# Optimization experiments

Hardware: AMD Instinct MI355X
Metric: run time of the kernel (lower is better)

## Reference

```python
import jax, jax.numpy as jnp
import numpy as np

EPS = 1e-7        # keras backend.epsilon()
TEMPERATURE = 0.1
MOMENTUM = 0.9
CENTROID_LR = 0.1
REPULSION_STRENGTH = 0.1
MIN_DISTANCE = 1.0

B, S, D = 8, 4096, 512
K = 512


def setup_inputs() -> dict:
    key = jax.random.key(0)
    kx, kc = jax.random.split(key)
    x = jax.random.normal(kx, (B, S, D), dtype=jnp.float32)
    # GlorotNormal for (K, D) centroid table
    glorot_std = float(np.sqrt(2.0 / (K + D)))
    centroids = jax.random.normal(kc, (K, D), dtype=jnp.float32) * glorot_std
    centroid_momentum = jnp.zeros((K, D), dtype=jnp.float32)
    return {"x": x, "centroids": centroids, "centroid_momentum": centroid_momentum}


def reference(x, centroids, centroid_momentum):
    # ---- flatten non-feature dims: (B, S, D) -> (N, D) ----
    flat = x.reshape(-1, x.shape[-1])                      # (N, D)

    # ---- squared Euclidean distances to centroids (GEMM form) ----
    x_sq = jnp.sum(flat * flat, axis=-1, keepdims=True)    # (N, 1)
    c_sq = jnp.sum(centroids * centroids, axis=-1)         # (K,)
    cross = flat @ centroids.T                             # (N, K)
    distances = x_sq + c_sq[None, :] - 2.0 * cross         # (N, K)

    # ---- temperature-scaled soft assignments (stable softmax w/ eps) ----
    scaled = -distances / TEMPERATURE
    scaled = scaled - jnp.max(scaled, axis=-1, keepdims=True)
    exp_d = jnp.exp(scaled)
    assignments = exp_d / (jnp.sum(exp_d, axis=-1, keepdims=True) + EPS)  # (N, K)

    # ---- soft K-means centroid targets ----
    sum_w = jnp.sum(assignments, axis=0)                   # (K,)
    weighted_sum = assignments.T @ flat                    # (K, D)
    new_centroids = weighted_sum / (sum_w[:, None] + EPS)  # (K, D)

    # ---- pairwise centroid repulsion ----
    diffs = centroids[:, None, :] - centroids[None, :, :]  # (K, K, D)
    sq_dist = jnp.sum(diffs * diffs, axis=-1)              # (K, K)
    dist = jnp.sqrt(sq_dist + EPS)
    rep_w = jnp.maximum(0.0, 1.0 - dist / MIN_DISTANCE)
    rep_scale = (REPULSION_STRENGTH * rep_w / (dist + EPS))[..., None]
    repulsion = jnp.sum(rep_scale * diffs, axis=1)         # (K, D)

    # ---- momentum update of centroids ----
    updates = new_centroids - centroids + repulsion
    mom_new = MOMENTUM * centroid_momentum + (1.0 - MOMENTUM) * updates
    centroids_new = centroids + CENTROID_LR * mom_new

    # ---- output: assignments reshaped to (B, S, K) ----
    out = assignments.reshape(x.shape[:-1] + (assignments.shape[-1],))
    return out, centroids_new, mom_new
```

## Files before the change

kernel.cpp:

```cpp
#include <hip/hip_runtime.h>
#include <hip/hip_bf16.h>

#define EPSF 1e-7f

typedef __attribute__((ext_vector_type(8))) short bf16x8;
typedef __attribute__((ext_vector_type(4))) float f32x4v;

__device__ inline ushort f2bf_bits(float x) {
    union { __hip_bfloat16 b; ushort u; } cv;
    cv.b = __float2bfloat16(x);
    return cv.u;
}
__device__ inline float bfbits2f(ushort u) {
    union { ushort u; __hip_bfloat16 b; } cv;
    cv.u = u;
    return __bfloat162float(cv.b);
}
__device__ inline void split2(float x, ushort& h, ushort& l) {
    h = f2bf_bits(x);
    l = f2bf_bits(x - bfbits2f(h));
}
__device__ inline uint4 pack8(const ushort* h) {
    uint4 p;
    p.x = (uint)h[0] | ((uint)h[1] << 16);
    p.y = (uint)h[2] | ((uint)h[3] << 16);
    p.z = (uint)h[4] | ((uint)h[5] << 16);
    p.w = (uint)h[6] | ((uint)h[7] << 16);
    return p;
}

__device__ inline void gload_lds16(const ushort* g, ushort* l) {
    __builtin_amdgcn_global_load_lds(
        (const __attribute__((address_space(1))) unsigned int*)g,
        (__attribute__((address_space(3))) unsigned int*)l, 16, 0, 0);
}

__global__ __launch_bounds__(256) void csqc_v3(const float* __restrict__ C,
                                               float* __restrict__ csq,
                                               ushort* __restrict__ Chl) {
    const int wave = threadIdx.x >> 6, lane = threadIdx.x & 63;
    const int row = blockIdx.x * 4 + wave;
    const int kc = lane >> 2, s = lane & 3;
    const float* p = C + row * 512 + lane * 8;
    float4 a = *(const float4*)p;
    float4 b = *(const float4*)(p + 4);
    float v[8] = {a.x, a.y, a.z, a.w, b.x, b.y, b.z, b.w};
    ushort h[8], l[8];
    float sqs = 0.f;
#pragma unroll
    for (int i = 0; i < 8; ++i) {
        sqs += v[i] * v[i];
        split2(v[i], h[i], l[i]);
    }
    ushort* base = Chl + (long)row * 1024 + kc * 64 + s * 8;
    *(uint4*)base = pack8(h);
    *(uint4*)(base + 32) = pack8(l);
#pragma unroll
    for (int off = 1; off < 64; off <<= 1) sqs += __shfl_xor(sqs, off, 64);
    if (lane == 0) csq[row] = sqs;
}

__global__ __launch_bounds__(512) void logsm(const float* __restrict__ X,
                                             const ushort* __restrict__ Chl,
                                             const float* __restrict__ csq,
                                             float* __restrict__ assign,
                                             ushort* __restrict__ Abf,
                                             ushort* __restrict__ Xh,
                                             float* __restrict__ sum_w) {
    __shared__ __align__(16) ushort sA[64 * 64];
    __shared__ __align__(16) ushort sB[512 * 64];
    __shared__ float rmaxs[64][4];
    __shared__ float rsums[64][4];
    __shared__ float swacc[512];
    const int tid = threadIdx.x;
    const int m0 = ((blockIdx.x & 7) * 64 + (blockIdx.x >> 3)) * 64;
    const int wid = tid >> 6, lane = tid & 63;
    const int wm = wid >> 2, wn = wid & 3;
    const int lrow = lane & 15, lkb = lane >> 4;
    swacc[tid] = 0.f;
    f32x4v acc[2][8] = {};

    const int ar = tid >> 3, aq = tid & 7;

#pragma unroll 1
    for (int kc = 0; kc < 16; ++kc) {
        __syncthreads();
        {
            float4 v = *(const float4*)(X + (long)(m0 + ar) * 512 + kc * 32 + aq * 4);
            ushort h[4], l[4];
            split2(v.x, h[0], l[0]);
            split2(v.y, h[1], l[1]);
            split2(v.z, h[2], l[2]);
            split2(v.w, h[3], l[3]);
            ushort4 hv = {h[0], h[1], h[2], h[3]};
            ushort4 lv = {l[0], l[1], l[2], l[3]};
            const int sh = (aq >> 1) ^ (ar & 7);
            const int slo = ((aq >> 1) + 4) ^ (ar & 7);
            *(ushort4*)&sA[ar * 64 + (sh << 3) + (aq & 1) * 4] = hv;
            *(ushort4*)&sA[ar * 64 + (slo << 3) + (aq & 1) * 4] = lv;
            *(ushort4*)(Xh + (long)(m0 + ar) * 512 + kc * 32 + aq * 4) = hv;
        }
#pragma unroll
        for (int i = 0; i < 8; ++i) {
            const int sl = i * 512 + tid;
            const int r = sl >> 3, j = sl & 7;
            const int s = j ^ (r & 7);
            gload_lds16(Chl + (long)r * 1024 + kc * 64 + s * 8,
                        &sB[(i * 512 + wid * 64) * 8]);
        }
        __syncthreads();
        bf16x8 ah[2], al[2];
#pragma unroll
        for (int mi = 0; mi < 2; ++mi) {
            const int R = wm * 32 + mi * 16 + lrow;
            ah[mi] = *(const bf16x8*)&sA[R * 64 + ((lkb ^ (R & 7)) << 3)];
            al[mi] = *(const bf16x8*)&sA[R * 64 + (((lkb + 4) ^ (R & 7)) << 3)];
        }
#pragma unroll
        for (int ni = 0; ni < 8; ++ni) {
            const int Rn = wn * 128 + ni * 16 + lrow;
            bf16x8 bh = *(const bf16x8*)&sB[Rn * 64 + ((lkb ^ (Rn & 7)) << 3)];
            bf16x8 bl = *(const bf16x8*)&sB[Rn * 64 + (((lkb + 4) ^ (Rn & 7)) << 3)];
#pragma unroll
            for (int mi = 0; mi < 2; ++mi) {
                acc[mi][ni] = __builtin_amdgcn_mfma_f32_16x16x32_bf16(ah[mi], bh, acc[mi][ni], 0, 0, 0);
                acc[mi][ni] = __builtin_amdgcn_mfma_f32_16x16x32_bf16(ah[mi], bl, acc[mi][ni], 0, 0, 0);
                acc[mi][ni] = __builtin_amdgcn_mfma_f32_16x16x32_bf16(al[mi], bh, acc[mi][ni], 0, 0, 0);
            }
        }
    }
    const int colb = wn * 128 + lrow;
    float cs[8];
#pragma unroll
    for (int ni = 0; ni < 8; ++ni) cs[ni] = csq[colb + ni * 16];
    float mx[2][4];
#pragma unroll
    for (int mi = 0; mi < 2; ++mi)
#pragma unroll
        for (int r = 0; r < 4; ++r) {
            float m = -3.0e38f;
#pragma unroll
            for (int ni = 0; ni < 8; ++ni) {
                float l = 2.0f * acc[mi][ni][r] - cs[ni];
                acc[mi][ni][r] = l;
                m = fmaxf(m, l);
            }
            mx[mi][r] = m;
        }
#pragma unroll
    for (int off = 1; off < 16; off <<= 1)
#pragma unroll
        for (int mi = 0; mi < 2; ++mi)
#pragma unroll
            for (int r = 0; r < 4; ++r) mx[mi][r] = fmaxf(mx[mi][r], __shfl_xor(mx[mi][r], off, 64));
    if (lrow == 0) {
#pragma unroll
        for (int mi = 0; mi < 2; ++mi)
#pragma unroll
            for (int r = 0; r < 4; ++r) rmaxs[wm * 32 + mi * 16 + lkb * 4 + r][wn] = mx[mi][r];
    }
    __syncthreads();
    float gmax[2][4];
#pragma unroll
    for (int mi = 0; mi < 2; ++mi)
#pragma unroll
        for (int r = 0; r < 4; ++r) {
            const int row = wm * 32 + mi * 16 + lkb * 4 + r;
            gmax[mi][r] = fmaxf(fmaxf(rmaxs[row][0], rmaxs[row][1]),
                                fmaxf(rmaxs[row][2], rmaxs[row][3]));
        }
    float sm[2][4] = {};
#pragma unroll
    for (int mi = 0; mi < 2; ++mi)
#pragma unroll
        for (int ni = 0; ni < 8; ++ni)
#pragma unroll
            for (int r = 0; r < 4; ++r) {
                float e = expf((acc[mi][ni][r] - gmax[mi][r]) * 10.0f);
                acc[mi][ni][r] = e;
                sm[mi][r] += e;
            }
#pragma unroll
    for (int off = 1; off < 16; off <<= 1)
#pragma unroll
        for (int mi = 0; mi < 2; ++mi)
#pragma unroll
            for (int r = 0; r < 4; ++r) sm[mi][r] += __shfl_xor(sm[mi][r], off, 64);
    if (lrow == 0) {
#pragma unroll
        for (int mi = 0; mi < 2; ++mi)
#pragma unroll
            for (int r = 0; r < 4; ++r) rsums[wm * 32 + mi * 16 + lkb * 4 + r][wn] = sm[mi][r];
    }
    __syncthreads();
    float inv[2][4];
#pragma unroll
    for (int mi = 0; mi < 2; ++mi)
#pragma unroll
        for (int r = 0; r < 4; ++r) {
            const int row = wm * 32 + mi * 16 + lkb * 4 + r;
            float t = rsums[row][0] + rsums[row][1] + rsums[row][2] + rsums[row][3];
            inv[mi][r] = 1.0f / (t + EPSF);
        }
    float csum[8] = {};
#pragma unroll
    for (int mi = 0; mi < 2; ++mi)
#pragma unroll
        for (int ni = 0; ni < 8; ++ni) {
            const int col = colb + ni * 16;
#pragma unroll
            for (int r = 0; r < 4; ++r) {
                const int row = wm * 32 + mi * 16 + lkb * 4 + r;
                float a = acc[mi][ni][r] * inv[mi][r];
                assign[(long)(m0 + row) * 512 + col] = a;
                Abf[(long)(m0 + row) * 512 + col] = f2bf_bits(a);
                csum[ni] += a;
            }
        }
#pragma unroll
    for (int off = 16; off < 64; off <<= 1)
#pragma unroll
        for (int ni = 0; ni < 8; ++ni) csum[ni] += __shfl_xor(csum[ni], off, 64);
    if (lkb == 0) {
#pragma unroll
        for (int ni = 0; ni < 8; ++ni) atomicAdd(&swacc[colb + ni * 16], csum[ni]);
    }
    __syncthreads();
    atomicAdd(&sum_w[tid], swacc[tid]);
}

__global__ __launch_bounds__(256) void gram_s_v3(const ushort* __restrict__ Chl,
                                                 const float* __restrict__ csq,
                                                 float* __restrict__ S,
                                                 float* __restrict__ rsum) {
    __shared__ __align__(16) ushort sA[128 * 64];
    __shared__ __align__(16) ushort sB[128 * 64];
    __shared__ float rs_s[128];
    const int tid = threadIdx.x;
    const int n0 = blockIdx.x * 128;
    const int m0 = blockIdx.y * 128;
    const int wid = tid >> 6, lane = tid & 63;
    const int wm = wid >> 1, wn = wid & 1;
    const int lrow = lane & 15, lkb = lane >> 4;
    f32x4v acc[4][4] = {};

#pragma unroll 1
    for (int kc = 0; kc < 16; ++kc) {
        __syncthreads();
#pragma unroll
        for (int i = 0; i < 4; ++i) {
            const int sl = wid * 256 + i * 64 + lane;
            const int r = sl >> 3, j = sl & 7;
            const int s = j ^ (r & 7);
            gload_lds16(Chl + (long)(m0 + r) * 1024 + kc * 64 + s * 8,
                        &sA[(wid * 256 + i * 64) * 8]);
            gload_lds16(Chl + (long)(n0 + r) * 1024 + kc * 64 + s * 8,
                        &sB[(wid * 256 + i * 64) * 8]);
        }
        __syncthreads();
        bf16x8 ah[4], al[4], bh[4], bl[4];
#pragma unroll
        for (int mi = 0; mi < 4; ++mi) {
            const int R = wm * 64 + mi * 16 + lrow;
            ah[mi] = *(const bf16x8*)&sA[R * 64 + ((lkb ^ (R & 7)) << 3)];
            al[mi] = *(const bf16x8*)&sA[R * 64 + (((lkb + 4) ^ (R & 7)) << 3)];
        }
#pragma unroll
        for (int ni = 0; ni < 4; ++ni) {
            const int R = wn * 64 + ni * 16 + lrow;
            bh[ni] = *(const bf16x8*)&sB[R * 64 + ((lkb ^ (R & 7)) << 3)];
            bl[ni] = *(const bf16x8*)&sB[R * 64 + (((lkb + 4) ^ (R & 7)) << 3)];
        }
#pragma unroll
        for (int mi = 0; mi < 4; ++mi)
#pragma unroll
            for (int ni = 0; ni < 4; ++ni) {
                acc[mi][ni] = __builtin_amdgcn_mfma_f32_16x16x32_bf16(ah[mi], bh[ni], acc[mi][ni], 0, 0, 0);
                acc[mi][ni] = __builtin_amdgcn_mfma_f32_16x16x32_bf16(ah[mi], bl[ni], acc[mi][ni], 0, 0, 0);
                acc[mi][ni] = __builtin_amdgcn_mfma_f32_16x16x32_bf16(al[mi], bh[ni], acc[mi][ni], 0, 0, 0);
            }
    }
    if (tid < 128) rs_s[tid] = 0.f;
    __syncthreads();
    const int colb = n0 + wn * 64 + lrow;
    float csj[4];
#pragma unroll
    for (int ni = 0; ni < 4; ++ni) csj[ni] = csq[colb + ni * 16];
#pragma unroll
    for (int mi = 0; mi < 4; ++mi) {
        const int rowb = m0 + wm * 64 + mi * 16 + lkb * 4;
#pragma unroll
        for (int r = 0; r < 4; ++r) {
            const int row = rowb + r;
            const float csi = csq[row];
            float rowpart = 0.f;
#pragma unroll
            for (int ni = 0; ni < 4; ++ni) {
                const int col = colb + ni * 16;
                float sq = csi + csj[ni] - 2.0f * acc[mi][ni][r];
                float dist = sqrtf(fmaxf(sq, 0.f) + EPSF);
                float w = fmaxf(0.f, 1.f - dist);
                float sval = (row == col) ? 0.f : (0.1f * w / (dist + EPSF));
                S[(long)row * 512 + col] = sval;
                rowpart += sval;
            }
            atomicAdd(&rs_s[row - m0], rowpart);
        }
    }
    __syncthreads();
    if (tid < 128) atomicAdd(&rsum[m0 + tid], rs_s[tid]);
}

__global__ __launch_bounds__(256) void wsum_v3(const ushort* __restrict__ Abf,
                                               const ushort* __restrict__ Xh,
                                               float* __restrict__ WSp) {
    __shared__ __align__(16) ushort sA[128 * 64];
    __shared__ __align__(16) ushort sB[128 * 64];
    const int tid = threadIdx.x;
    const int lin = blockIdx.x + blockIdx.y * 4 + blockIdx.z * 16;
    const int T = (lin & 7) * 64 + (lin >> 3);
    const int k0 = (T & 3) * 128;
    const int d0 = ((T >> 2) & 3) * 128;
    const int zc = T >> 4;
    const long n0 = (long)zc * 1024;
    const int wid = tid >> 6, lane = tid & 63;
    const int wm = wid >> 1, wn = wid & 1;
    const int lrow = lane & 15, lkb = lane >> 4;
    f32x4v acc[4][4] = {};

    for (int nc = 0; nc < 1024; nc += 64) {
        __syncthreads();
#pragma unroll
        for (int it = 0; it < 4; ++it) {
            const int idx = it * 256 + tid;
            const int c = idx & 127;
            const int no = idx >> 7;
            const long nb = n0 + nc + (long)no * 8;
            const int dd = d0 + c;
            ushort ha[8], hx[8];
#pragma unroll
            for (int jj = 0; jj < 8; ++jj) {
                ha[jj] = Abf[(nb + jj) * 512 + k0 + c];
                hx[jj] = Xh[(nb + jj) * 512 + dd];
            }
            const int sl = no ^ (c & 7);
            *(uint4*)&sA[c * 64 + sl * 8] = pack8(ha);
            *(uint4*)&sB[c * 64 + sl * 8] = pack8(hx);
        }
        __syncthreads();
#pragma unroll
        for (int kk = 0; kk < 2; ++kk) {
            const int j = kk * 4 + lkb;
            bf16x8 af[4], bfv[4];
#pragma unroll
            for (int mi = 0; mi < 4; ++mi) {
                const int R = wm * 64 + mi * 16 + lrow;
                af[mi] = *(const bf16x8*)&sA[R * 64 + ((j ^ (R & 7)) << 3)];
            }
#pragma unroll
            for (int ni = 0; ni < 4; ++ni) {
                const int R = wn * 64 + ni * 16 + lrow;
                bfv[ni] = *(const bf16x8*)&sB[R * 64 + ((j ^ (R & 7)) << 3)];
            }
#pragma unroll
            for (int mi = 0; mi < 4; ++mi)
#pragma unroll
                for (int ni = 0; ni < 4; ++ni)
                    acc[mi][ni] = __builtin_amdgcn_mfma_f32_16x16x32_bf16(af[mi], bfv[ni], acc[mi][ni], 0, 0, 0);
        }
    }
    float* dst = WSp + (size_t)zc * 262144;
#pragma unroll
    for (int mi = 0; mi < 4; ++mi) {
        const int k = k0 + wm * 64 + mi * 16 + lkb * 4;
#pragma unroll
        for (int ni = 0; ni < 4; ++ni) {
            const int d = d0 + wn * 64 + ni * 16 + lrow;
#pragma unroll
            for (int r = 0; r < 4; ++r)
                dst[(k + r) * 512 + d] = acc[mi][ni][r];
        }
    }
}

__global__ __launch_bounds__(256) void apply_update(const float* __restrict__ Cent,
                                                    const float* __restrict__ Mom,
                                                    const float* __restrict__ S,
                                                    const float* __restrict__ rsum,
                                                    const float* __restrict__ WSp,
                                                    const float* __restrict__ sum_w,
                                                    float* __restrict__ outC,
                                                    float* __restrict__ outM) {
    const int i = blockIdx.x;
    __shared__ float srow[512];
    __shared__ int nz;
    const int tid = threadIdx.x;
    if (tid == 0) nz = 0;
    __syncthreads();
    float2 sv = *(const float2*)(S + (long)i * 512 + tid * 2);
    srow[tid * 2] = sv.x;
    srow[tid * 2 + 1] = sv.y;
    if (sv.x != 0.f || sv.y != 0.f) nz = 1;
    __syncthreads();
    const float rs = rsum[i];
    const float invw = 1.0f / (sum_w[i] + EPSF);
    const int d0 = tid * 2;
    float ws0 = 0.f, ws1 = 0.f;
#pragma unroll 4
    for (int z = 0; z < 32; ++z) {
        float2 w = *(const float2*)(WSp + (size_t)z * 262144 + (long)i * 512 + d0);
        ws0 += w.x;
        ws1 += w.y;
    }
    float sc0 = 0.f, sc1 = 0.f;
    if (nz) {
        for (int j = 0; j < 512; ++j) {
            const float s = srow[j];
            if (s != 0.f) {
                sc0 += s * Cent[(long)j * 512 + d0];
                sc1 += s * Cent[(long)j * 512 + d0 + 1];
            }
        }
    }
    float2 ci = *(const float2*)(Cent + (long)i * 512 + d0);
    float2 mo = *(const float2*)(Mom + (long)i * 512 + d0);
    float rep0 = rs * ci.x - sc0;
    float rep1 = rs * ci.y - sc1;
    float mn0 = 0.9f * mo.x + 0.1f * (ws0 * invw - ci.x + rep0);
    float mn1 = 0.9f * mo.y + 0.1f * (ws1 * invw - ci.y + rep1);
    float2 om = {mn0, mn1};
    float2 oc = {ci.x + 0.1f * mn0, ci.y + 0.1f * mn1};
    *(float2*)(outM + (long)i * 512 + d0) = om;
    *(float2*)(outC + (long)i * 512 + d0) = oc;
}

__global__ __launch_bounds__(256) void csq_only(const float* __restrict__ C,
                                                float* __restrict__ csq) {
    const int wave = threadIdx.x >> 6, lane = threadIdx.x & 63;
    const int row = blockIdx.x * 4 + wave;
    const float* p = C + row * 512 + lane * 8;
    float4 a = *(const float4*)p;
    float4 b = *(const float4*)(p + 4);
    float s = a.x * a.x + a.y * a.y + a.z * a.z + a.w * a.w +
              b.x * b.x + b.y * b.y + b.z * b.z + b.w * b.w;
#pragma unroll
    for (int off = 1; off < 64; off <<= 1) s += __shfl_xor(s, off, 64);
    if (lane == 0) csq[row] = s;
}

__global__ __launch_bounds__(256) void logits_mfma(const float* __restrict__ X,
                                                   const float* __restrict__ Cm,
                                                   const float* __restrict__ csq,
                                                   float* __restrict__ L) {
    __shared__ ushort sAh[128][64];
    __shared__ ushort sAl[128][64];
    __shared__ ushort sBh[128][64];
    __shared__ ushort sBl[128][64];
    const int tid = threadIdx.x;
    const int m0 = blockIdx.x * 128;
    const int n0 = blockIdx.y * 128;
    const int wid = tid >> 6, lane = tid & 63;
    const int wm = wid >> 1, wn = wid & 1;
    const int lrow = lane & 15;
    const int lkb = lane >> 4;
    f32x4v acc[4][4] = {};
    for (int k0 = 0; k0 < 512; k0 += 64) {
        __syncthreads();
#pragma unroll
        for (int s = 0; s < 8; ++s) {
            const int idx = s * 256 + tid;
            const int r = idx >> 4;
            const int c4 = (idx & 15) << 2;
            const int e = c4 ^ ((r & 7) << 3);
            float4 va = *(const float4*)(X + (long)(m0 + r) * 512 + k0 + c4);
            ushort4 hh, ll;
            split2(va.x, hh.x, ll.x);
            split2(va.y, hh.y, ll.y);
            split2(va.z, hh.z, ll.z);
            split2(va.w, hh.w, ll.w);
            *(ushort4*)&sAh[r][e] = hh;
            *(ushort4*)&sAl[r][e] = ll;
            float4 vb = *(const float4*)(Cm + (long)(n0 + r) * 512 + k0 + c4);
            split2(vb.x, hh.x, ll.x);
            split2(vb.y, hh.y, ll.y);
            split2(vb.z, hh.z, ll.z);
            split2(vb.w, hh.w, ll.w);
            *(ushort4*)&sBh[r][e] = hh;
            *(ushort4*)&sBl[r][e] = ll;
        }
        __syncthreads();
#pragma unroll
        for (int kk = 0; kk < 2; ++kk) {
            const int ebase = kk * 32 + lkb * 8;
            bf16x8 ah[4], al[4], bh[4], bl[4];
#pragma unroll
            for (int mi = 0; mi < 4; ++mi) {
                const int R = wm * 64 + mi * 16 + lrow;
                const int e = ebase ^ ((R & 7) << 3);
                ah[mi] = *(const bf16x8*)&sAh[R][e];
                al[mi] = *(const bf16x8*)&sAl[R][e];
            }
#pragma unroll
            for (int ni = 0; ni < 4; ++ni) {
                const int Rn = wn * 64 + ni * 16 + lrow;
                const int e = ebase ^ ((Rn & 7) << 3);
                bh[ni] = *(const bf16x8*)&sBh[Rn][e];
                bl[ni] = *(const bf16x8*)&sBl[Rn][e];
            }
#pragma unroll
            for (int mi = 0; mi < 4; ++mi)
#pragma unroll
                for (int ni = 0; ni < 4; ++ni) {
                    acc[mi][ni] = __builtin_amdgcn_mfma_f32_16x16x32_bf16(ah[mi], bh[ni], acc[mi][ni], 0, 0, 0);
                    acc[mi][ni] = __builtin_amdgcn_mfma_f32_16x16x32_bf16(ah[mi], bl[ni], acc[mi][ni], 0, 0, 0);
                    acc[mi][ni] = __builtin_amdgcn_mfma_f32_16x16x32_bf16(al[mi], bh[ni], acc[mi][ni], 0, 0, 0);
                }
        }
    }
    const int colb = n0 + wn * 64 + lrow;
    float cs[4];
#pragma unroll
    for (int ni = 0; ni < 4; ++ni) cs[ni] = csq[colb + ni * 16];
#pragma unroll
    for (int mi = 0; mi < 4; ++mi) {
        const int rowb = m0 + wm * 64 + mi * 16 + lkb * 4;
#pragma unroll
        for (int r = 0; r < 4; ++r) {
            float* Lp = L + (long)(rowb + r) * 512 + colb;
#pragma unroll
            for (int ni = 0; ni < 4; ++ni)
                Lp[ni * 16] = 2.0f * acc[mi][ni][r] - cs[ni];
        }
    }
}

__global__ __launch_bounds__(256) void softmax_rows(float* __restrict__ L,
                                                    float* __restrict__ sum_w,
                                                    ushort* __restrict__ Abf) {
    __shared__ float swacc[512];
    const int tid = threadIdx.x;
    for (int i = tid; i < 512; i += 256) swacc[i] = 0.f;
    __syncthreads();
    const int wave = tid >> 6, lane = tid & 63;
    float racc[8] = {};
    for (int r = blockIdx.x * 4 + wave; r < 32768; r += 2048) {
        float* p = L + (long)r * 512 + lane * 8;
        float4 v0 = *(float4*)p;
        float4 v1 = *(float4*)(p + 4);
        float v[8] = {v0.x, v0.y, v0.z, v0.w, v1.x, v1.y, v1.z, v1.w};
        float m = v[0];
#pragma unroll
        for (int i = 1; i < 8; ++i) m = fmaxf(m, v[i]);
#pragma unroll
        for (int off = 1; off < 64; off <<= 1) m = fmaxf(m, __shfl_xor(m, off, 64));
        float e[8], s = 0.f;
#pragma unroll
        for (int i = 0; i < 8; ++i) {
            e[i] = expf((v[i] - m) * 10.0f);
            s += e[i];
        }
#pragma unroll
        for (int off = 1; off < 64; off <<= 1) s += __shfl_xor(s, off, 64);
        const float inv = 1.0f / (s + EPSF);
        ushort eb[8];
#pragma unroll
        for (int i = 0; i < 8; ++i) {
            e[i] *= inv;
            racc[i] += e[i];
            eb[i] = f2bf_bits(e[i]);
        }
        float4 o0 = {e[0], e[1], e[2], e[3]};
        float4 o1 = {e[4], e[5], e[6], e[7]};
        *(float4*)p = o0;
        *(float4*)(p + 4) = o1;
        if (Abf) *(uint4*)(Abf + (long)r * 512 + lane * 8) = pack8(eb);
    }
#pragma unroll
    for (int i = 0; i < 8; ++i) atomicAdd(&swacc[lane * 8 + i], racc[i]);
    __syncthreads();
    for (int i = tid; i < 512; i += 256) atomicAdd(&sum_w[i], swacc[i]);
}

__global__ __launch_bounds__(256) void gemm_wsum(const float* __restrict__ A,
                                                 const float* __restrict__ X,
                                                 float* __restrict__ WS) {
    __shared__ float As[16][64];
    __shared__ float Xs[16][64];
    const int tid = threadIdx.x;
    const int tx = tid & 15, ty = tid >> 4;
    const int lrow = tid >> 4;
    const int lcol = (tid & 15) << 2;
    const int k0 = blockIdx.x * 64;
    const int d0 = blockIdx.y * 64;
    const int n0 = blockIdx.z * 1024;
    float acc[4][4] = {};
    for (int nc = 0; nc < 1024; nc += 16) {
        const long nrow = n0 + nc + lrow;
        float4 av = *(const float4*)(A + nrow * 512 + k0 + lcol);
        float4 xv = *(const float4*)(X + nrow * 512 + d0 + lcol);
        __syncthreads();
        *(float4*)&As[lrow][lcol] = av;
        *(float4*)&Xs[lrow][lcol] = xv;
        __syncthreads();
#pragma unroll
        for (int nn = 0; nn < 16; ++nn) {
            float4 a = *(const float4*)&As[nn][ty << 2];
            float4 x = *(const float4*)&Xs[nn][tx << 2];
            float aa[4] = {a.x, a.y, a.z, a.w};
            float xx[4] = {x.x, x.y, x.z, x.w};
#pragma unroll
            for (int i = 0; i < 4; ++i)
#pragma unroll
                for (int j = 0; j < 4; ++j) acc[i][j] += aa[i] * xx[j];
        }
    }
#pragma unroll
    for (int i = 0; i < 4; ++i)
#pragma unroll
        for (int j = 0; j < 4; ++j)
            atomicAdd(&WS[(k0 + (ty << 2) + i) * 512 + d0 + (tx << 2) + j], acc[i][j]);
}

__global__ __launch_bounds__(256) void repulse_update(const float* __restrict__ Cent,
                                                      const float* __restrict__ Mom,
                                                      const float* __restrict__ csq,
                                                      const float* __restrict__ WS,
                                                      const float* __restrict__ sum_w,
                                                      float* __restrict__ outC,
                                                      float* __restrict__ outM) {
    const int i = blockIdx.x;
    __shared__ float ci[512];
    __shared__ float rep[512];
    const int tid = threadIdx.x, wave = tid >> 6, lane = tid & 63;
    for (int d = tid; d < 512; d += 256) {
        ci[d] = Cent[i * 512 + d];
        rep[d] = 0.f;
    }
    __syncthreads();
    float cil[8];
#pragma unroll
    for (int m = 0; m < 8; ++m) cil[m] = ci[lane * 8 + m];
    const float csqi = csq[i];
    float racc[8] = {};
    for (int j = wave; j < 512; j += 4) {
        if (j == i) continue;
        const float* cj = Cent + j * 512 + lane * 8;
        float4 c0 = *(const float4*)cj;
        float4 c1 = *(const float4*)(cj + 4);
        float cjl[8] = {c0.x, c0.y, c0.z, c0.w, c1.x, c1.y, c1.z, c1.w};
        float dot = 0.f;
#pragma unroll
        for (int m = 0; m < 8; ++m) dot += cil[m] * cjl[m];
#pragma unroll
        for (int off = 1; off < 64; off <<= 1) dot += __shfl_xor(dot, off, 64);
        float sq = csqi + csq[j] - 2.f * dot;
        float dist = sqrtf(fmaxf(sq, 0.f) + EPSF);
        float w = fmaxf(0.f, 1.f - dist);
        float scale = 0.1f * w / (dist + EPSF);
#pragma unroll
        for (int m = 0; m < 8; ++m) racc[m] += scale * (cil[m] - cjl[m]);
    }
#pragma unroll
    for (int m = 0; m < 8; ++m) atomicAdd(&rep[lane * 8 + m], racc[m]);
    __syncthreads();
    const float invw = 1.0f / (sum_w[i] + EPSF);
    for (int d = tid; d < 512; d += 256) {
        float nc = WS[i * 512 + d] * invw;
        float upd = nc - ci[d] + rep[d];
        float mn = 0.9f * Mom[i * 512 + d] + 0.1f * upd;
        outM[i * 512 + d] = mn;
        outC[i * 512 + d] = ci[d] + 0.1f * mn;
    }
}

extern "C" void kernel_launch(void* const* d_in, const int* in_sizes, int n_in,
                              void* d_out, int out_size, void* d_ws, size_t ws_size,
                              hipStream_t stream) {
    const float* X = (const float*)d_in[0];
    const float* C = (const float*)d_in[1];
    const float* M = (const float*)d_in[2];
    float* out = (float*)d_out;
    float* assign = out;
    float* outC = out + 16777216;
    float* outM = outC + 262144;

    char* wsb = (char*)d_ws;
    const size_t MB = 1024ull * 1024ull;
    float* WS = (float*)wsb;
    float* sum_w = (float*)(wsb + 1 * MB);
    float* rsum = (float*)(wsb + 1 * MB + 2048);
    float* csq = (float*)(wsb + 1 * MB + 4096);
    ushort* Chl = (ushort*)(wsb + 2 * MB);
    float* S = (float*)(wsb + 3 * MB);
    float* WSp = (float*)(wsb + 4 * MB);
    ushort* Xh = (ushort*)(wsb + 36 * MB);
    ushort* Abf = (ushort*)(wsb + 100 * MB);
    const size_t NEED = 132 * MB;

    if (ws_size >= NEED) {
        hipMemsetAsync(wsb + 1 * MB, 0, 4096, stream);
        csqc_v3<<<128, 256, 0, stream>>>(C, csq, Chl);
        gram_s_v3<<<dim3(4, 4), 256, 0, stream>>>(Chl, csq, S, rsum);
        logsm<<<512, 512, 0, stream>>>(X, Chl, csq, assign, Abf, Xh, sum_w);
        wsum_v3<<<dim3(4, 4, 32), 256, 0, stream>>>(Abf, Xh, WSp);
        apply_update<<<512, 256, 0, stream>>>(C, M, S, rsum, WSp, sum_w, outC, outM);
    } else {
        hipMemsetAsync(d_ws, 0, 1 * MB + 8192, stream);
        csq_only<<<128, 256, 0, stream>>>(C, csq);
        logits_mfma<<<dim3(256, 4), 256, 0, stream>>>(X, C, csq, assign);
        softmax_rows<<<512, 256, 0, stream>>>(assign, sum_w, nullptr);
        gemm_wsum<<<dim3(8, 8, 32), 256, 0, stream>>>(assign, X, WS);
        repulse_update<<<512, 256, 0, stream>>>(C, M, csq, WS, sum_w, outC, outM);
    }
}
```

Measured before the change: 146.6 us.

## Software-pipeline global loads in GEMM kernels with register prefetch and LDS double-buffering

After: 176.3 us. 1.2x slower.

```diff
diff --git a/kernel.cpp b/kernel.cpp
--- a/kernel.cpp
+++ b/kernel.cpp
@@ -81,12 +81,13 @@
     f32x4v acc[2][8] = {};
 
     const int ar = tid >> 3, aq = tid & 7;
+    const float* xrow = X + (long)(m0 + ar) * 512 + aq * 4;
+    float4 v = *(const float4*)xrow;
 
 #pragma unroll 1
     for (int kc = 0; kc < 16; ++kc) {
         __syncthreads();
         {
-            float4 v = *(const float4*)(X + (long)(m0 + ar) * 512 + kc * 32 + aq * 4);
             ushort h[4], l[4];
             split2(v.x, h[0], l[0]);
             split2(v.y, h[1], l[1]);
@@ -108,6 +109,7 @@
             gload_lds16(Chl + (long)r * 1024 + kc * 64 + s * 8,
                         &sB[(i * 512 + wid * 64) * 8]);
         }
+        if (kc < 15) v = *(const float4*)(xrow + (kc + 1) * 32);
         __syncthreads();
         bf16x8 ah[2], al[2];
 #pragma unroll
@@ -314,8 +316,8 @@
 __global__ __launch_bounds__(256) void wsum_v3(const ushort* __restrict__ Abf,
                                                const ushort* __restrict__ Xh,
                                                float* __restrict__ WSp) {
-    __shared__ __align__(16) ushort sA[128 * 64];
-    __shared__ __align__(16) ushort sB[128 * 64];
+    __shared__ __align__(16) ushort sA[2][128 * 64];
+    __shared__ __align__(16) ushort sB[2][128 * 64];
     const int tid = threadIdx.x;
     const int lin = blockIdx.x + blockIdx.y * 4 + blockIdx.z * 16;
     const int T = (lin & 7) * 64 + (lin >> 3);
@@ -328,25 +330,43 @@
     const int lrow = lane & 15, lkb = lane >> 4;
     f32x4v acc[4][4] = {};
 
-    for (int nc = 0; nc < 1024; nc += 64) {
-        __syncthreads();
-#pragma unroll
-        for (int it = 0; it < 4; ++it) {
-            const int idx = it * 256 + tid;
-            const int c = idx & 127;
-            const int no = idx >> 7;
-            const long nb = n0 + nc + (long)no * 8;
-            const int dd = d0 + c;
-            ushort ha[8], hx[8];
-#pragma unroll
-            for (int jj = 0; jj < 8; ++jj) {
-                ha[jj] = Abf[(nb + jj) * 512 + k0 + c];
-                hx[jj] = Xh[(nb + jj) * 512 + dd];
-            }
-            const int sl = no ^ (c & 7);
-            *(uint4*)&sA[c * 64 + sl * 8] = pack8(ha);
-            *(uint4*)&sB[c * 64 + sl * 8] = pack8(hx);
-        }
+    const int c0_ = tid & 127, no0 = tid >> 7;
+    ushort ha[4][8], hx[4][8];
+
+#define WSUM_LOAD(NCOFF)                                                      \
+    {                                                                          \
+        _Pragma("unroll")                                                      \
+        for (int it = 0; it < 4; ++it) {                                       \
+            const int idx = it * 256 + tid;                                    \
+            const int c = idx & 127;                                           \
+            const int no = idx >> 7;                                           \
+            const long nb = n0 + (NCOFF) + (long)no * 8;                       \
+            _Pragma("unroll")                                                  \
+            for (int jj = 0; jj < 8; ++jj) {                                   \
+                ha[it][jj] = Abf[(nb + jj) * 512 + k0 + c];                    \
+                hx[it][jj] = Xh[(nb + jj) * 512 + d0 + c];                     \
+            }                                                                  \
+        }                                                                      \
+    }
+#define WSUM_WRITE(B)                                                         \
+    {                                                                          \
+        _Pragma("unroll")                                                      \
+        for (int it = 0; it < 4; ++it) {                                       \
+            const int idx = it * 256 + tid;                                    \
+            const int c = idx & 127;                                           \
+            const int no = idx >> 7;                                           \
+            const int sl = no ^ (c & 7);                                       \
+            *(uint4*)&sA[(B)][c * 64 + sl * 8] = pack8(ha[it]);                \
+            *(uint4*)&sB[(B)][c * 64 + sl * 8] = pack8(hx[it]);                \
+        }                                                                      \
+    }
+
+    WSUM_LOAD(0);
+    WSUM_WRITE(0);
+    int cur = 0;
+#pragma unroll 1
+    for (int nc = 0; nc < 16; ++nc) {
+        if (nc < 15) WSUM_LOAD((nc + 1) * 64);
         __syncthreads();
 #pragma unroll
         for (int kk = 0; kk < 2; ++kk) {
@@ -355,12 +375,12 @@
 #pragma unroll
             for (int mi = 0; mi < 4; ++mi) {
                 const int R = wm * 64 + mi * 16 + lrow;
-                af[mi] = *(const bf16x8*)&sA[R * 64 + ((j ^ (R & 7)) << 3)];
+                af[mi] = *(const bf16x8*)&sA[cur][R * 64 + ((j ^ (R & 7)) << 3)];
             }
 #pragma unroll
             for (int ni = 0; ni < 4; ++ni) {
                 const int R = wn * 64 + ni * 16 + lrow;
-                bfv[ni] = *(const bf16x8*)&sB[R * 64 + ((j ^ (R & 7)) << 3)];
+                bfv[ni] = *(const bf16x8*)&sB[cur][R * 64 + ((j ^ (R & 7)) << 3)];
             }
 #pragma unroll
             for (int mi = 0; mi < 4; ++mi)
@@ -368,6 +388,8 @@
                 for (int ni = 0; ni < 4; ++ni)
                     acc[mi][ni] = __builtin_amdgcn_mfma_f32_16x16x32_bf16(af[mi], bfv[ni], acc[mi][ni], 0, 0, 0);
         }
+        if (nc < 15) WSUM_WRITE(cur ^ 1);
+        cur ^= 1;
     }
     float* dst = WSp + (size_t)zc * 262144;
 #pragma unroll
@@ -381,6 +403,8 @@
                 dst[(k + r) * 512 + d] = acc[mi][ni][r];
         }
     }
+#undef WSUM_LOAD
+#undef WSUM_WRITE
 }
 
 __global__ __launch_bounds__(256) void apply_update(const float* __restrict__ Cent,
```
